# Optimization experiments

Measured on AMD Instinct MI355X. Metric: run time of the kernel, lower is better.

Reference implementation:

```python
import jax, jax.numpy as jnp
import numpy as np

B, T, M, P = 64, 2048, 512, 512


def setup_inputs() -> dict:
    key = jax.random.key(0)
    ks = jax.random.split(key, 9)
    s = 0.02
    return {
        "hidden_state": jax.random.normal(ks[0], (B, P), jnp.float32),
        "cell_state": jax.random.normal(ks[1], (B, P), jnp.float32),
        "encoder_h": jax.random.normal(ks[2], (B, T, M), jnp.float32),
        # Dense W_d: (2p -> m)
        "W_d": jax.random.normal(ks[3], (2 * P, M), jnp.float32) * s,
        "b_wd": jnp.zeros((M,), jnp.float32),
        # Dense U_d: (m -> m)
        "U_d": jax.random.normal(ks[4], (M, M), jnp.float32) * s,
        "b_ud": jnp.zeros((M,), jnp.float32),
        # Dense v_d: (m -> 1)
        "v_d": jax.random.normal(ks[5], (M, 1), jnp.float32) * s,
        "b_vd": jnp.zeros((1,), jnp.float32),
    }


def reference(hidden_state, cell_state, encoder_h, W_d, b_wd, U_d, b_ud, v_d, b_vd):
    # W_d(RepeatVector(T)(concat([d, s]))): the Dense is applied to the same
    # (B, 2p) vector at every time step, so compute it once and broadcast.
    ds = jnp.concatenate([hidden_state, cell_state], axis=-1)          # (B, 2p)
    ds_proj = ds @ W_d + b_wd                                          # (B, m)
    enc_proj = jnp.einsum('btm,mn->btn', encoder_h, U_d) + b_ud        # (B, T, m)
    e = jnp.tanh(ds_proj[:, None, :] + enc_proj)                       # (B, T, m)
    l = e @ v_d + b_vd                                                 # (B, T, 1)
    return jax.nn.softmax(l, axis=1)                                   # softmax over T
```

## Files before the change

kernel.cpp:

```cpp
#include <hip/hip_runtime.h>
#include <cstdint>
#include <cstddef>

#define ROWS 131072
#define NCOLS 512

typedef float  floatx4 __attribute__((ext_vector_type(4)));
typedef short  shortx8 __attribute__((ext_vector_type(8)));

__device__ __forceinline__ short f2bf_rne(float f) {
  unsigned u = __float_as_uint(f);
  unsigned r = u + 0x7FFFu + ((u >> 16) & 1u);
  return (short)(r >> 16);
}

__device__ __forceinline__ unsigned pack_bf_trunc(float lo, float hi) {
  return __builtin_amdgcn_perm(__float_as_uint(hi), __float_as_uint(lo), 0x07060302u);
}

#define GLOAD_LDS16(gptr, lptr)                                                 \
  __builtin_amdgcn_global_load_lds(                                             \
      (const __attribute__((address_space(1))) void*)(gptr),                    \
      (__attribute__((address_space(3))) void*)(lptr), 16, 0, 0)

extern "C" __global__ __launch_bounds__(256) void prep_kernel(
    const float* __restrict__ hidden, const float* __restrict__ cell,
    const float* __restrict__ W_d, const float* __restrict__ b_wd,
    const float* __restrict__ U_d, const float* __restrict__ b_ud,
    float* __restrict__ S, short* __restrict__ U_T, float* __restrict__ lzero)
{
  int bx = blockIdx.x, tid = threadIdx.x;
  if (bx < 128) {
    int idx = bx * 256 + tid;
    int b = idx >> 9, n = idx & 511;
    const float* h = hidden + b * 512;
    const float* c = cell   + b * 512;
    float acc = b_wd[n] + b_ud[n];
    for (int k = 0; k < 512; ++k) acc = fmaf(h[k], W_d[k * 512 + n], acc);
    for (int k = 0; k < 512; ++k) acc = fmaf(c[k], W_d[(k + 512) * 512 + n], acc);
    S[idx] = acc;
  } else if (bx < 384) {
    int idx = (bx - 128) * 1024 + tid * 4;
    int n = idx >> 9, k0 = idx & 511;
    unsigned lo = (unsigned short)f2bf_rne(U_d[(size_t)(k0 + 0) * 512 + n]) |
                  ((unsigned)(unsigned short)f2bf_rne(U_d[(size_t)(k0 + 1) * 512 + n]) << 16);
    unsigned hi = (unsigned short)f2bf_rne(U_d[(size_t)(k0 + 2) * 512 + n]) |
                  ((unsigned)(unsigned short)f2bf_rne(U_d[(size_t)(k0 + 3) * 512 + n]) << 16);
    uint2 w; w.x = lo; w.y = hi;
    *(uint2*)(U_T + idx) = w;
  } else {
    int idx = ((bx - 384) * 256 + tid) * 4;
    floatx4 z = {0.f, 0.f, 0.f, 0.f};
    *(floatx4*)(lzero + idx) = z;
  }
}

extern "C" __global__ __launch_bounds__(256) void attn_gemm(
    const float* __restrict__ A, const short* __restrict__ UT,
    const float* __restrict__ S, const float* __restrict__ vd,
    float* __restrict__ lout)
{
  __shared__ float Asw[128 * 32];
  __shared__ short Bs[128 * 32];

  const int tid = threadIdx.x;
  const int bx  = blockIdx.x;
  const int xcd = bx & 7;
  const int k7  = bx >> 3;
  const int rb  = xcd * 128 + (k7 >> 2);
  const int cb  = k7 & 3;
  const int row0 = rb * 128;
  const int col0 = cb * 128;
  const int wave = tid >> 6;
  const int lane = tid & 63;
  const int wr = wave >> 1, wc = wave & 1;
  const int q = lane >> 4, l15 = lane & 15;

  const float* asrc[4];
#pragma unroll
  for (int j = 0; j < 4; ++j) {
    int c = wave * 4 + j;
    int m = c * 8 + (lane >> 3);
    int pl = (lane & 7) ^ (m & 7);
    asrc[j] = A + (size_t)(row0 + m) * 512 + pl * 4;
  }
  const short* bsrc[2];
#pragma unroll
  for (int j = 0; j < 2; ++j) {
    int c = wave * 2 + j;
    int n = c * 16 + (lane >> 2);
    int ks = (lane & 3) * 8;
    bsrc[j] = UT + (size_t)(col0 + n) * 512 + ks;
  }

  int aoff0[4], aoff1[4], boff[4];
#pragma unroll
  for (int t = 0; t < 4; ++t) {
    int m = wr * 64 + t * 16 + l15;
    int s = m & 7;
    aoff0[t] = m * 32 + (((2 * q) ^ s) << 2);
    aoff1[t] = m * 32 + ((((2 * q) | 1) ^ s) << 2);
    int n = wc * 64 + t * 16 + l15;
    boff[t] = n * 32 + q * 8;
  }

  floatx4 acc[4][4];
#pragma unroll
  for (int i = 0; i < 4; ++i)
#pragma unroll
    for (int j = 0; j < 4; ++j)
      acc[i][j] = (floatx4){0.f, 0.f, 0.f, 0.f};

  for (int kk = 0; kk < 512; kk += 32) {
    __syncthreads();
#pragma unroll
    for (int j = 0; j < 4; ++j)
      GLOAD_LDS16(asrc[j] + kk, &Asw[(wave * 4 + j) * 256]);
#pragma unroll
    for (int j = 0; j < 2; ++j)
      GLOAD_LDS16(bsrc[j] + kk, &Bs[(wave * 2 + j) * 512]);
    __syncthreads();

    shortx8 af[4], bf[4];
#pragma unroll
    for (int t = 0; t < 4; ++t) {
      floatx4 a0 = *(const floatx4*)(Asw + aoff0[t]);
      floatx4 a1 = *(const floatx4*)(Asw + aoff1[t]);
      union { shortx8 v; unsigned u[4]; } fu;
      fu.u[0] = pack_bf_trunc(a0.x, a0.y);
      fu.u[1] = pack_bf_trunc(a0.z, a0.w);
      fu.u[2] = pack_bf_trunc(a1.x, a1.y);
      fu.u[3] = pack_bf_trunc(a1.z, a1.w);
      af[t] = fu.v;
      bf[t] = *(const shortx8*)(Bs + boff[t]);
    }
#pragma unroll
    for (int tr = 0; tr < 4; ++tr)
#pragma unroll
      for (int tc = 0; tc < 4; ++tc)
        acc[tr][tc] = __builtin_amdgcn_mfma_f32_16x16x32_bf16(
            af[tr], bf[tc], acc[tr][tc], 0, 0, 0);
  }

  const int bb = row0 >> 11;
  const float* Srow = S + bb * 512;
#pragma unroll
  for (int tr = 0; tr < 4; ++tr) {
#pragma unroll
    for (int r = 0; r < 4; ++r) {
      float ssum = 0.f;
#pragma unroll
      for (int tc = 0; tc < 4; ++tc) {
        int n = col0 + wc * 64 + tc * 16 + l15;
        float x = acc[tr][tc][r] + Srow[n];
        x = fminf(15.f, fmaxf(-15.f, x));
        float e2 = __expf(2.f * x);
        float e = (e2 - 1.f) / (e2 + 1.f);
        ssum += e * vd[n];
      }
      ssum += __shfl_xor(ssum, 1);
      ssum += __shfl_xor(ssum, 2);
      ssum += __shfl_xor(ssum, 4);
      ssum += __shfl_xor(ssum, 8);
      if (l15 == 0) {
        int row = row0 + wr * 64 + tr * 16 + q * 4 + r;
        atomicAdd(lout + row, ssum);
      }
    }
  }
}

extern "C" __global__ __launch_bounds__(256) void softmax_t(float* __restrict__ l)
{
  int b = blockIdx.x, tid = threadIdx.x;
  int wave = tid >> 6, lane = tid & 63;
  float* row = l + (size_t)b * 2048;
  float v[8];
  float mx = -3.4e38f;
#pragma unroll
  for (int i = 0; i < 8; ++i) { v[i] = row[tid + i * 256]; mx = fmaxf(mx, v[i]); }
#pragma unroll
  for (int m = 1; m < 64; m <<= 1) mx = fmaxf(mx, __shfl_xor(mx, m));
  __shared__ float red[8];
  if (lane == 0) red[wave] = mx;
  __syncthreads();
  mx = fmaxf(fmaxf(red[0], red[1]), fmaxf(red[2], red[3]));
  float s = 0.f;
#pragma unroll
  for (int i = 0; i < 8; ++i) { v[i] = __expf(v[i] - mx); s += v[i]; }
#pragma unroll
  for (int m = 1; m < 64; m <<= 1) s += __shfl_xor(s, m);
  if (lane == 0) red[4 + wave] = s;
  __syncthreads();
  s = red[4] + red[5] + red[6] + red[7];
  float inv = 1.f / s;
#pragma unroll
  for (int i = 0; i < 8; ++i) row[tid + i * 256] = v[i] * inv;
}

extern "C" void kernel_launch(void* const* d_in, const int* in_sizes, int n_in,
                              void* d_out, int out_size, void* d_ws, size_t ws_size,
                              hipStream_t stream) {
  const float* hidden = (const float*)d_in[0];
  const float* cell   = (const float*)d_in[1];
  const float* enc    = (const float*)d_in[2];
  const float* W_d    = (const float*)d_in[3];
  const float* b_wd   = (const float*)d_in[4];
  const float* U_d    = (const float*)d_in[5];
  const float* b_ud   = (const float*)d_in[6];
  const float* v_d    = (const float*)d_in[7];
  float* out = (float*)d_out;
  float* S   = (float*)d_ws;
  short* UT  = (short*)((char*)d_ws + 32768 * sizeof(float));

  hipLaunchKernelGGL(prep_kernel, dim3(512), dim3(256), 0, stream,
                     hidden, cell, W_d, b_wd, U_d, b_ud, S, UT, out);
  hipLaunchKernelGGL(attn_gemm, dim3(4096), dim3(256), 0, stream,
                     enc, UT, S, v_d, out);
  hipLaunchKernelGGL(softmax_t, dim3(64), dim3(256), 0, stream, out);
}
```

Baseline: 531.4 us.

## Double-buffer GEMM with 256x256 tiles, register-staged A conversion, and pre-swizzled U

The attention GEMM moves from 128x128 tiles with 256 threads to 256x256 tiles with 512 threads and double-buffered LDS. The fp32 encoder tile is prefetched into registers and converted to bf16 once on the LDS store instead of at every fragment read, and U is written by the prep kernel already tiled and swizzled so it can be copied straight into LDS. Explicit waitcnt, sched barriers and setprio overlap the next tile's loads with the MFMAs. The aim is to hide global latency, halve A's LDS footprint and reuse each loaded tile across more output. In exchange it uses more registers (launch bounds 512,2) and depends on fragile hand-written synchronisation.

```diff
diff --git a/kernel.cpp b/kernel.cpp
--- a/kernel.cpp
+++ b/kernel.cpp
@@ -2,8 +2,6 @@
 #include <cstdint>
 #include <cstddef>
 
-#define ROWS 131072
-#define NCOLS 512
 
 typedef float  floatx4 __attribute__((ext_vector_type(4)));
 typedef short  shortx8 __attribute__((ext_vector_type(8)));
@@ -23,11 +21,15 @@
       (const __attribute__((address_space(1))) void*)(gptr),                    \
       (__attribute__((address_space(3))) void*)(lptr), 16, 0, 0)
 
+#define SB() __builtin_amdgcn_sched_barrier(0)
+#define WAIT_VM(n) asm volatile("s_waitcnt vmcnt(" #n ")" ::: "memory")
+#define WAIT_LGKM0() asm volatile("s_waitcnt lgkmcnt(0)" ::: "memory")
+
 extern "C" __global__ __launch_bounds__(256) void prep_kernel(
     const float* __restrict__ hidden, const float* __restrict__ cell,
     const float* __restrict__ W_d, const float* __restrict__ b_wd,
     const float* __restrict__ U_d, const float* __restrict__ b_ud,
-    float* __restrict__ S, short* __restrict__ U_T, float* __restrict__ lzero)
+    float* __restrict__ S, short* __restrict__ UT, float* __restrict__ lzero)
 {
   int bx = blockIdx.x, tid = threadIdx.x;
   if (bx < 128) {
@@ -41,13 +43,22 @@
     S[idx] = acc;
   } else if (bx < 384) {
     int idx = (bx - 128) * 1024 + tid * 4;
-    int n = idx >> 9, k0 = idx & 511;
-    unsigned lo = (unsigned short)f2bf_rne(U_d[(size_t)(k0 + 0) * 512 + n]) |
-                  ((unsigned)(unsigned short)f2bf_rne(U_d[(size_t)(k0 + 1) * 512 + n]) << 16);
-    unsigned hi = (unsigned short)f2bf_rne(U_d[(size_t)(k0 + 2) * 512 + n]) |
-                  ((unsigned)(unsigned short)f2bf_rne(U_d[(size_t)(k0 + 3) * 512 + n]) << 16);
+    int cbp = idx >> 17;
+    int r2  = idx & 131071;
+    int ktp = r2 >> 13;
+    int sI  = r2 & 8191;
+    int n    = sI >> 5;
+    int slot = (sI >> 3) & 3;
+    int b16  = sI & 7;
+    int kb16 = slot ^ (n & 3);
+    int k0 = ktp * 32 + (kb16 << 3) + b16;
+    int ng = cbp * 256 + n;
+    unsigned lo = (unsigned short)f2bf_rne(U_d[(size_t)(k0 + 0) * 512 + ng]) |
+                  ((unsigned)(unsigned short)f2bf_rne(U_d[(size_t)(k0 + 1) * 512 + ng]) << 16);
+    unsigned hi = (unsigned short)f2bf_rne(U_d[(size_t)(k0 + 2) * 512 + ng]) |
+                  ((unsigned)(unsigned short)f2bf_rne(U_d[(size_t)(k0 + 3) * 512 + ng]) << 16);
     uint2 w; w.x = lo; w.y = hi;
-    *(uint2*)(U_T + idx) = w;
+    *(uint2*)(UT + idx) = w;
   } else {
     int idx = ((bx - 384) * 256 + tid) * 4;
     floatx4 z = {0.f, 0.f, 0.f, 0.f};
@@ -55,115 +66,178 @@
   }
 }
 
-extern "C" __global__ __launch_bounds__(256) void attn_gemm(
+extern "C" __global__ __launch_bounds__(512, 2) void attn_gemm(
     const float* __restrict__ A, const short* __restrict__ UT,
     const float* __restrict__ S, const float* __restrict__ vd,
     float* __restrict__ lout)
 {
-  __shared__ float Asw[128 * 32];
-  __shared__ short Bs[128 * 32];
+  __shared__ short As[2][8192];
+  __shared__ short Bs[2][8192];
 
   const int tid = threadIdx.x;
   const int bx  = blockIdx.x;
   const int xcd = bx & 7;
-  const int k7  = bx >> 3;
-  const int rb  = xcd * 128 + (k7 >> 2);
-  const int cb  = k7 & 3;
-  const int row0 = rb * 128;
-  const int col0 = cb * 128;
+  const int wg  = xcd * 128 + (bx >> 3);
+  const int cb  = wg & 1;
+  const int rb  = wg >> 1;
+  const int row0 = rb << 8;
+  const int col0 = cb << 8;
   const int wave = tid >> 6;
   const int lane = tid & 63;
-  const int wr = wave >> 1, wc = wave & 1;
+  const int wr = wave >> 2, wc = wave & 3;
   const int q = lane >> 4, l15 = lane & 15;
 
   const float* asrc[4];
+  int awr[4];
 #pragma unroll
   for (int j = 0; j < 4; ++j) {
-    int c = wave * 4 + j;
-    int m = c * 8 + (lane >> 3);
-    int pl = (lane & 7) ^ (m & 7);
-    asrc[j] = A + (size_t)(row0 + m) * 512 + pl * 4;
+    int row = j * 64 + (tid >> 3);
+    int ch  = tid & 7;
+    asrc[j] = A + (size_t)(row0 + row) * 512 + ch * 4;
+    awr[j]  = row * 32 + ((((ch >> 1) ^ (row & 3)) << 3) + (ch & 1) * 4);
   }
   const short* bsrc[2];
+  int bdst[2];
 #pragma unroll
   for (int j = 0; j < 2; ++j) {
-    int c = wave * 2 + j;
-    int n = c * 16 + (lane >> 2);
-    int ks = (lane & 3) * 8;
-    bsrc[j] = UT + (size_t)(col0 + n) * 512 + ks;
-  }
-
-  int aoff0[4], aoff1[4], boff[4];
-#pragma unroll
-  for (int t = 0; t < 4; ++t) {
-    int m = wr * 64 + t * 16 + l15;
-    int s = m & 7;
-    aoff0[t] = m * 32 + (((2 * q) ^ s) << 2);
-    aoff1[t] = m * 32 + ((((2 * q) | 1) ^ s) << 2);
-    int n = wc * 64 + t * 16 + l15;
-    boff[t] = n * 32 + q * 8;
-  }
-
-  floatx4 acc[4][4];
-#pragma unroll
-  for (int i = 0; i < 4; ++i)
+    int ws = j * 8 + wave;
+    bsrc[j] = UT + cb * 131072 + ws * 512 + lane * 8;
+    bdst[j] = ws * 512;
+  }
+
+  int aoff[8], boff[4];
+#pragma unroll
+  for (int tr = 0; tr < 8; ++tr) {
+    int row = wr * 128 + tr * 16 + l15;
+    aoff[tr] = row * 32 + ((q ^ (row & 3)) << 3);
+  }
+#pragma unroll
+  for (int tc = 0; tc < 4; ++tc) {
+    int n = wc * 64 + tc * 16 + l15;
+    boff[tc] = n * 32 + ((q ^ (n & 3)) << 3);
+  }
+
+  floatx4 acc[8][4];
+#pragma unroll
+  for (int i = 0; i < 8; ++i)
 #pragma unroll
     for (int j = 0; j < 4; ++j)
       acc[i][j] = (floatx4){0.f, 0.f, 0.f, 0.f};
 
-  for (int kk = 0; kk < 512; kk += 32) {
-    __syncthreads();
-#pragma unroll
-    for (int j = 0; j < 4; ++j)
-      GLOAD_LDS16(asrc[j] + kk, &Asw[(wave * 4 + j) * 256]);
-#pragma unroll
-    for (int j = 0; j < 2; ++j)
-      GLOAD_LDS16(bsrc[j] + kk, &Bs[(wave * 2 + j) * 512]);
-    __syncthreads();
-
-    shortx8 af[4], bf[4];
-#pragma unroll
-    for (int t = 0; t < 4; ++t) {
-      floatx4 a0 = *(const floatx4*)(Asw + aoff0[t]);
-      floatx4 a1 = *(const floatx4*)(Asw + aoff1[t]);
-      union { shortx8 v; unsigned u[4]; } fu;
-      fu.u[0] = pack_bf_trunc(a0.x, a0.y);
-      fu.u[1] = pack_bf_trunc(a0.z, a0.w);
-      fu.u[2] = pack_bf_trunc(a1.x, a1.y);
-      fu.u[3] = pack_bf_trunc(a1.z, a1.w);
-      af[t] = fu.v;
-      bf[t] = *(const shortx8*)(Bs + boff[t]);
-    }
+  floatx4 areg[4];
+
+#pragma unroll
+  for (int j = 0; j < 4; ++j) areg[j] = *(const floatx4*)(asrc[j]);
+  SB();
+#pragma unroll
+  for (int j = 0; j < 2; ++j) GLOAD_LDS16(bsrc[j], &Bs[0][bdst[j]]);
+  SB();
+  WAIT_VM(2); SB();
+#pragma unroll
+  for (int j = 0; j < 4; ++j) {
+    uint2 w;
+    w.x = pack_bf_trunc(areg[j].x, areg[j].y);
+    w.y = pack_bf_trunc(areg[j].z, areg[j].w);
+    *(uint2*)(&As[0][0] + awr[j]) = w;
+  }
+  SB();
+#pragma unroll
+  for (int j = 0; j < 4; ++j) areg[j] = *(const floatx4*)(asrc[j] + 32);
+  SB();
+  WAIT_VM(4); SB();
+  WAIT_LGKM0(); SB();
+  __builtin_amdgcn_s_barrier(); SB();
+
+#pragma unroll
+  for (int t = 0; t < 16; ++t) {
+    const int cur = t & 1;
+    const short* Ab = &As[cur][0];
+    const short* Bb = &Bs[cur][0];
+    shortx8 af[4], bfr[4];
+#pragma unroll
+    for (int tc = 0; tc < 4; ++tc) bfr[tc] = *(const shortx8*)(Bb + boff[tc]);
+#pragma unroll
+    for (int tr = 0; tr < 4; ++tr) af[tr] = *(const shortx8*)(Ab + aoff[tr]);
+    WAIT_LGKM0(); SB();
+    __builtin_amdgcn_s_setprio(1);
 #pragma unroll
     for (int tr = 0; tr < 4; ++tr)
 #pragma unroll
       for (int tc = 0; tc < 4; ++tc)
         acc[tr][tc] = __builtin_amdgcn_mfma_f32_16x16x32_bf16(
-            af[tr], bf[tc], acc[tr][tc], 0, 0, 0);
-  }
-
-  const int bb = row0 >> 11;
+            af[tr], bfr[tc], acc[tr][tc], 0, 0, 0);
+    __builtin_amdgcn_s_setprio(0);
+    SB();
+    if (t < 15) {
+      WAIT_VM(0); SB();
+      short* An = &As[cur ^ 1][0];
+#pragma unroll
+      for (int j = 0; j < 4; ++j) {
+        uint2 w;
+        w.x = pack_bf_trunc(areg[j].x, areg[j].y);
+        w.y = pack_bf_trunc(areg[j].z, areg[j].w);
+        *(uint2*)(An + awr[j]) = w;
+      }
+#pragma unroll
+      for (int j = 0; j < 2; ++j)
+        GLOAD_LDS16(bsrc[j] + (t + 1) * 8192, &Bs[cur ^ 1][bdst[j]]);
+      SB();
+      if (t < 14) {
+#pragma unroll
+        for (int j = 0; j < 4; ++j)
+          areg[j] = *(const floatx4*)(asrc[j] + (t + 2) * 32);
+      }
+      SB();
+    }
+#pragma unroll
+    for (int tr = 0; tr < 4; ++tr) af[tr] = *(const shortx8*)(Ab + aoff[tr + 4]);
+    WAIT_LGKM0(); SB();
+    __builtin_amdgcn_s_setprio(1);
+#pragma unroll
+    for (int tr = 0; tr < 4; ++tr)
+#pragma unroll
+      for (int tc = 0; tc < 4; ++tc)
+        acc[tr + 4][tc] = __builtin_amdgcn_mfma_f32_16x16x32_bf16(
+            af[tr], bfr[tc], acc[tr + 4][tc], 0, 0, 0);
+    __builtin_amdgcn_s_setprio(0);
+    SB();
+    if (t < 15) {
+      if (t < 14) { WAIT_VM(4); }
+      else        { WAIT_VM(0); }
+      SB();
+      __builtin_amdgcn_s_barrier();
+      SB();
+    }
+  }
+
+  const int bb = rb >> 3;
   const float* Srow = S + bb * 512;
-#pragma unroll
-  for (int tr = 0; tr < 4; ++tr) {
+  float sv[4], vv[4];
+#pragma unroll
+  for (int tc = 0; tc < 4; ++tc) {
+    int n = col0 + wc * 64 + tc * 16 + l15;
+    sv[tc] = Srow[n];
+    vv[tc] = vd[n];
+  }
+#pragma unroll
+  for (int tr = 0; tr < 8; ++tr) {
 #pragma unroll
     for (int r = 0; r < 4; ++r) {
       float ssum = 0.f;
 #pragma unroll
       for (int tc = 0; tc < 4; ++tc) {
-        int n = col0 + wc * 64 + tc * 16 + l15;
-        float x = acc[tr][tc][r] + Srow[n];
+        float x = acc[tr][tc][r] + sv[tc];
         x = fminf(15.f, fmaxf(-15.f, x));
         float e2 = __expf(2.f * x);
         float e = (e2 - 1.f) / (e2 + 1.f);
-        ssum += e * vd[n];
+        ssum += e * vv[tc];
       }
       ssum += __shfl_xor(ssum, 1);
       ssum += __shfl_xor(ssum, 2);
       ssum += __shfl_xor(ssum, 4);
       ssum += __shfl_xor(ssum, 8);
       if (l15 == 0) {
-        int row = row0 + wr * 64 + tr * 16 + q * 4 + r;
+        int row = row0 + wr * 128 + tr * 16 + q * 4 + r;
         atomicAdd(lout + row, ssum);
       }
     }
@@ -215,7 +289,7 @@
 
   hipLaunchKernelGGL(prep_kernel, dim3(512), dim3(256), 0, stream,
                      hidden, cell, W_d, b_wd, U_d, b_ud, S, UT, out);
-  hipLaunchKernelGGL(attn_gemm, dim3(4096), dim3(256), 0, stream,
+  hipLaunchKernelGGL(attn_gemm, dim3(1024), dim3(512), 0, stream,
                      enc, UT, S, v_d, out);
   hipLaunchKernelGGL(softmax_t, dim3(64), dim3(256), 0, stream, out);
 }
```

Measured after the change: 492.8 us. 7.3% less time.
